# Optimization experiments

Hardware: AMD Instinct MI355X
Metric: run time of the kernel (lower is better)

The kernel has to match this reference:

```python
import jax, jax.numpy as jnp
import numpy as np

PRE_NMS_THRESH = 0.05
PRE_NMS_TOP_N = 200
NMS_THRESH = 0.5
FPN_POST_NMS_TOP_N = 100
MIN_SIZE = 0.0
NUM_CLASSES = 2
C = NUM_CLASSES - 1
NB = 2
STRIDES = (8, 16, 32, 64, 128)
HS = (100, 50, 25, 13, 7)
WS = (128, 64, 32, 16, 8)
IMG_H, IMG_W = 800, 1024
MAXV = 8  # max #vertices of quad-clipped-by-quad polygon


def _shoelace_fixed(V, n):
    # area of polygon stored in fixed buffer V[MAXV,2] with n valid vertices
    a = jnp.asarray(0.0, V.dtype)
    for k in range(MAXV):
        nxt = jnp.where(jnp.equal(k, n - 1), 0, k + 1)
        term = V[k, 0] * V[nxt, 1] - V[nxt, 0] * V[k, 1]
        a = a + jnp.where(k < n, term, 0.0)
    return 0.5 * jnp.abs(a)


def _quad_area(Q):  # Q: [4,2]
    x, y = Q[:, 0], Q[:, 1]
    return 0.5 * jnp.abs(jnp.sum(x * jnp.roll(y, -1) - jnp.roll(x, -1) * y))


def _clip_halfplane(V, n, p1, p2, orient):
    # Sutherland-Hodgman clip of polygon (V,n) against directed edge p1->p2
    d = p2 - p1

    def side(p):
        return orient * (d[0] * (p[1] - p1[1]) - d[1] * (p[0] - p1[0]))

    out = jnp.zeros((MAXV, 2), V.dtype)
    cnt = jnp.int32(0)
    for k in range(MAXV):
        cur = V[k]
        prev = V[jnp.where(jnp.equal(k, 0), n - 1, k - 1)]
        sc = side(cur)
        sp = side(prev)
        cur_in = sc >= 0.0
        prev_in = sp >= 0.0
        denom = sp - sc
        t = sp / jnp.where(jnp.abs(denom) > 1e-9, denom, 1e-9)
        ip = prev + t * (cur - prev)
        valid = k < n
        emit_ip = valid & (cur_in != prev_in)
        out = jnp.where(emit_ip, out.at[cnt].set(ip, mode='drop'), out)
        cnt = cnt + emit_ip.astype(jnp.int32)
        emit_cur = valid & cur_in
        out = jnp.where(emit_cur, out.at[cnt].set(cur, mode='drop'), out)
        cnt = cnt + emit_cur.astype(jnp.int32)
    return out, cnt


def _poly_inter_area(A, B):  # A,B: [4,2] convex quads
    sB = jnp.sum(B[:, 0] * jnp.roll(B[:, 1], -1) - jnp.roll(B[:, 0], -1) * B[:, 1])
    orient = jnp.where(sB >= 0.0, 1.0, -1.0)
    V = jnp.zeros((MAXV, 2), A.dtype).at[:4].set(A)
    n = jnp.int32(4)
    for e in range(4):
        V, n = _clip_halfplane(V, n, B[e], B[(e + 1) % 4], orient)
    return _shoelace_fixed(V, n)


def _process_level(loc, cls_l, reg_l, image_sizes):
    Nb, Cc, H, W = cls_l.shape
    # (N,C,H,W) -> (N,HW*C) with index = (h*W+w)*C + c (matches permute/reshape)
    scores = jax.nn.sigmoid(cls_l.transpose(0, 2, 3, 1).reshape(Nb, H * W * Cc))
    cand = scores > PRE_NMS_THRESH
    masked = jnp.where(cand, scores, 0.0)
    k = min(PRE_NMS_TOP_N, H * W * Cc)
    vals, idx = jax.lax.top_k(masked, k)
    loc_idx = idx // Cc
    labels = idx % Cc + 1
    regr = reg_l.transpose(0, 2, 3, 1).reshape(Nb, H * W, 8)
    reg_g = jnp.take_along_axis(regr, loc_idx[..., None], axis=1)  # [Nb,k,8]
    loc_g = loc[loc_idx]  # [Nb,k,2]
    poly = jnp.tile(loc_g, (1, 1, 4)) - reg_g  # (x-r0, y-r1, ..., x-r6, y-r7)
    hh = image_sizes[:, 0].astype(poly.dtype)[:, None, None]
    ww = image_sizes[:, 1].astype(poly.dtype)[:, None, None]
    xs = jnp.clip(poly[..., 0::2], 0.0, ww - 1.0)
    ys = jnp.clip(poly[..., 1::2], 0.0, hh - 1.0)
    poly = jnp.stack([xs, ys], axis=-1).reshape(Nb, k, 8)
    valid = vals > PRE_NMS_THRESH
    bw = xs.max(-1) - xs.min(-1)
    bh = ys.max(-1) - ys.min(-1)
    valid = valid & (bw >= MIN_SIZE) & (bh >= MIN_SIZE)
    sc = jnp.where(valid, jnp.sqrt(vals), 0.0)
    return poly, sc, labels, valid


def _nms_single(poly, scores, labels, valid):
    T = scores.shape[0]
    order = jnp.argsort(-scores)
    poly = poly[order]
    scores = scores[order]
    labels = labels[order]
    valid = valid[order]
    quads = poly.reshape(T, 4, 2)

    def pairwise_iou(q):
        inter = jax.vmap(jax.vmap(_poly_inter_area, (None, 0)), (0, None))(q, q)
        areas = jax.vmap(_quad_area)(q)
        union = areas[:, None] + areas[None, :] - inter
        return inter / jnp.maximum(union, 1e-9)

    # IoU only feeds boolean suppression decisions -> no gradient flows through it
    iou = jax.lax.stop_gradient(pairwise_iou(quads))
    ar = jnp.arange(T)

    def body(i, keep):
        sup = (iou[i] > NMS_THRESH) & (ar > i)
        return jnp.where(keep[i], keep & ~sup, keep)

    keep = jax.lax.stop_gradient(jax.lax.fori_loop(0, T, body, valid))
    final = jnp.where(keep, scores, -1.0)
    top_s, top_i = jax.lax.top_k(final, FPN_POST_NMS_TOP_N)
    ok = top_s > 0.0
    return poly[top_i], jnp.where(ok, top_s, 0.0), labels[top_i], ok


def _forward(locs, clss, regs, image_sizes):
    parts = [_process_level(l, c, r, image_sizes) for l, c, r in zip(locs, clss, regs)]
    poly = jnp.concatenate([p[0] for p in parts], axis=1)
    sc = jnp.concatenate([p[1] for p in parts], axis=1)
    lab = jnp.concatenate([p[2] for p in parts], axis=1)
    val = jnp.concatenate([p[3] for p in parts], axis=1)
    return jax.vmap(_nms_single)(poly, sc, lab, val)


def setup_inputs() -> dict:
    key = jax.random.key(0)
    inp = {}
    k = key
    for i, (h, w, s) in enumerate(zip(HS, WS, STRIDES)):
        k, k1, k2, k3 = jax.random.split(k, 4)
        sx = jnp.arange(w, dtype=jnp.float32) * s + s // 2
        sy = jnp.arange(h, dtype=jnp.float32) * s + s // 2
        yy, xx = jnp.meshgrid(sy, sx, indexing='ij')
        inp[f'locations_l{i}'] = jnp.stack([xx.reshape(-1), yy.reshape(-1)], axis=1)
        inp[f'box_cls_l{i}'] = jax.random.normal(k1, (NB, C, h, w), dtype=jnp.float32)
        inp[f'box_reg_l{i}'] = jax.random.normal(k2, (NB, 8, h, w), dtype=jnp.float32) * (2.0 * s)
        inp[f'centerness_l{i}'] = jax.random.normal(k3, (NB, 1, h, w), dtype=jnp.float32)
    inp['image_sizes'] = jnp.array([[IMG_H, IMG_W]] * NB, dtype=jnp.int32)
    return inp


def reference(locations_l0, locations_l1, locations_l2, locations_l3, locations_l4,
              box_cls_l0, box_cls_l1, box_cls_l2, box_cls_l3, box_cls_l4,
              box_reg_l0, box_reg_l1, box_reg_l2, box_reg_l3, box_reg_l4,
              centerness_l0, centerness_l1, centerness_l2, centerness_l3, centerness_l4,
              image_sizes):
    # centerness is accepted but unused, matching the original module's forward
    locs = [locations_l0, locations_l1, locations_l2, locations_l3, locations_l4]
    clss = [box_cls_l0, box_cls_l1, box_cls_l2, box_cls_l3, box_cls_l4]
    regs = [box_reg_l0, box_reg_l1, box_reg_l2, box_reg_l3, box_reg_l4]
    boxes, scores, labels, valid = _forward(locs, clss, regs, image_sizes)
    return boxes, scores, labels, valid
```

## Files before the change

### kernel.cpp

```cpp
#include <hip/hip_runtime.h>

#pragma clang fp contract(off)

#define T_CAND 856
#define NW 14
#define BSC 128
#define NSH 16
#define HSTR 513

__device__ const int d_HW[5]  = {12800, 3200, 800, 208, 56};
__device__ const int d_K[5]   = {200, 200, 200, 200, 56};
__device__ const int d_OFF[5] = {0, 200, 400, 600, 800};

struct LevelPtrs {
  const float* loc[5];
  const float* cls[5];
  const float* reg[5];
  const int*   img;
};

__device__ __forceinline__ unsigned long long readlane64(unsigned long long v, int lane) {
  const unsigned lo = (unsigned)__builtin_amdgcn_readlane((int)(unsigned)(v & 0xFFFFFFFFULL), lane);
  const unsigned hi = (unsigned)__builtin_amdgcn_readlane((int)(unsigned)(v >> 32), lane);
  return ((unsigned long long)hi << 32) | lo;
}
__device__ __forceinline__ unsigned long long rfl64(unsigned long long v) {
  const unsigned lo = (unsigned)__builtin_amdgcn_readfirstlane((int)(unsigned)(v & 0xFFFFFFFFULL));
  const unsigned hi = (unsigned)__builtin_amdgcn_readfirstlane((int)(unsigned)(v >> 32));
  return ((unsigned long long)hi << 32) | lo;
}

__global__ __launch_bounds__(1024) void topk_kernel(LevelPtrs P,
    float* __restrict__ candPoly, float* __restrict__ candSc, unsigned* __restrict__ candValid) {
  __shared__ unsigned hist[NSH * HSTR];
  __shared__ unsigned histT[512];
  __shared__ __align__(16) unsigned long long gbuf[1024];
  __shared__ int gcount;
  __shared__ int cutB;
  const int blk = blockIdx.x;
  const int b = blk / 5, l = blk % 5;
  const int HW = d_HW[l], K = d_K[l], OFF = d_OFF[l];
  const float* cls = P.cls[l] + (size_t)b * HW;
  const float* reg = P.reg[l] + (size_t)b * 8 * HW;
  const float* loc = P.loc[l];
  const int tid = threadIdx.x;

  for (int t = tid; t < NSH * HSTR; t += 1024) hist[t] = 0u;
  if (tid == 0) gcount = 0;
  __syncthreads();

  const int sh = (tid >> 2) & (NSH - 1);
  for (int idx = tid; idx < HW; idx += 1024) {
    const float x = cls[idx];
    const float s = (float)(1.0 / (1.0 + exp(-(double)x)));
    const float m = (s > 0.05f) ? s : 0.0f;
    atomicAdd(&hist[sh * HSTR + (__float_as_uint(m) >> 21)], 1u);
  }
  __syncthreads();
  for (int t = tid; t < 512; t += 1024) {
    unsigned sum = 0;
#pragma unroll
    for (int h = 0; h < NSH; ++h) sum += hist[h * HSTR + t];
    histT[t] = sum;
  }
  __syncthreads();
  if (tid == 0) {
    int acc = 0, bx = 511;
    for (; bx >= 0; --bx) { acc += (int)histT[bx]; if (acc >= K) break; }
    cutB = (bx < 0) ? 0 : bx;
  }
  __syncthreads();

  const int cb = cutB;
  for (int idx = tid; idx < HW; idx += 1024) {
    const float x = cls[idx];
    const float s = (float)(1.0 / (1.0 + exp(-(double)x)));
    const float m = (s > 0.05f) ? s : 0.0f;
    const unsigned kb = __float_as_uint(m);
    if ((int)(kb >> 21) >= cb) {
      const int pos = atomicAdd(&gcount, 1);
      if (pos < 1024)
        gbuf[pos] = ((unsigned long long)kb << 32)
                  | (unsigned long long)(0xFFFFFFFFu - (unsigned)idx);
    }
  }
  __syncthreads();
  const int G = min(gcount, 1024);
  if (tid < 4 && G + tid < 1024) gbuf[G + tid] = 0ULL;
  __syncthreads();

  if (tid < G) {
    const unsigned long long my = gbuf[tid];
    const int G4 = (G + 3) & ~3;
    int rank = 0;
    const ulonglong2* g2 = (const ulonglong2*)gbuf;
    for (int j = 0; j < G4 / 2; j += 2) {
      const ulonglong2 a = g2[j], c = g2[j + 1];
      rank += (a.x > my) ? 1 : 0;
      rank += (a.y > my) ? 1 : 0;
      rank += (c.x > my) ? 1 : 0;
      rank += (c.y > my) ? 1 : 0;
    }
    if (rank < K) {
      const float val = __uint_as_float((unsigned)(my >> 32));
      const int idx = (int)(0xFFFFFFFFu - (unsigned)(my & 0xFFFFFFFFULL));
      const float hh = (float)P.img[b * 2 + 0];
      const float ww = (float)P.img[b * 2 + 1];
      const float xmax = ww - 1.0f, ymax = hh - 1.0f;
      const float lx = loc[idx * 2 + 0], ly = loc[idx * 2 + 1];
      const int go = b * T_CAND + OFF + rank;
#pragma unroll
      for (int q = 0; q < 4; ++q) {
        const float rx = reg[(2 * q + 0) * HW + idx];
        const float ry = reg[(2 * q + 1) * HW + idx];
        const float pxv = fminf(fmaxf(lx - rx, 0.0f), xmax);
        const float pyv = fminf(fmaxf(ly - ry, 0.0f), ymax);
        candPoly[go * 8 + 2 * q + 0] = pxv;
        candPoly[go * 8 + 2 * q + 1] = pyv;
      }
      const bool v = (val > 0.05f);
      candSc[go]    = v ? sqrtf(val) : 0.0f;
      candValid[go] = v ? 1u : 0u;
    }
  }
}

__global__ __launch_bounds__(1024) void sort_kernel(
    const float* __restrict__ candPoly, const float* __restrict__ candSc,
    const unsigned* __restrict__ candValid,
    float* __restrict__ sPoly, float* __restrict__ sSc, unsigned* __restrict__ sValid) {
  __shared__ __align__(16) unsigned long long key[T_CAND];
  const int b = blockIdx.x, tid = threadIdx.x;
  float sc = 0.0f;
  if (tid < T_CAND) {
    sc = candSc[b * T_CAND + tid];
    key[tid] = ((unsigned long long)__float_as_uint(sc) << 32)
             | (unsigned long long)(0xFFFFFFFFu - (unsigned)tid);
  }
  __syncthreads();
  if (tid < T_CAND) {
    const unsigned long long my = key[tid];
    int rank = 0;
    const ulonglong2* k2 = (const ulonglong2*)key;
    for (int j = 0; j < T_CAND / 2; j += 2) {
      const ulonglong2 a = k2[j], c = k2[j + 1];
      rank += (a.x > my) ? 1 : 0;
      rank += (a.y > my) ? 1 : 0;
      rank += (c.x > my) ? 1 : 0;
      rank += (c.y > my) ? 1 : 0;
    }
    sSc[b * T_CAND + rank]    = sc;
    sValid[b * T_CAND + rank] = candValid[b * T_CAND + tid];
    const float4* src = (const float4*)(candPoly + (size_t)(b * T_CAND + tid) * 8);
    float4* dst = (float4*)(sPoly + (size_t)(b * T_CAND + rank) * 8);
    dst[0] = src[0];
    dst[1] = src[1];
  }
}

__global__ __launch_bounds__(BSC) void iou_kernel(const float* __restrict__ sPoly,
                                                  const unsigned* __restrict__ sValid,
                                                  unsigned long long* __restrict__ MT) {
  __shared__ float VX[2][8][BSC];
  __shared__ float VY[2][8][BSC];
  const int i = blockIdx.y, b = blockIdx.z;
  const int tid = threadIdx.x;
  if (blockIdx.x * BSC + (BSC - 1) <= (unsigned)i) {
    if ((tid & 63) == 0) {
      const int jw = blockIdx.x * (BSC / 64) + (tid >> 6);
      MT[((size_t)b * NW + jw) * T_CAND + i] = 0ULL;
    }
    return;
  }
  if (sValid[b * T_CAND + i] == 0u) return;
  const int j = blockIdx.x * BSC + tid;
  const float4* Ap4 = (const float4*)(sPoly + (size_t)(b * T_CAND + i) * 8);
  const float4 a01 = Ap4[0], a23 = Ap4[1];
  const float ax0 = a01.x, ay0 = a01.y, ax1 = a01.z, ay1 = a01.w,
              ax2 = a23.x, ay2 = a23.y, ax3 = a23.z, ay3 = a23.w;
  const int jc = (j < T_CAND) ? j : (T_CAND - 1);
  const float4* Bp4 = (const float4*)(sPoly + (size_t)(b * T_CAND + jc) * 8);
  const float4 b01 = Bp4[0], b23 = Bp4[1];
  const float bx0 = b01.x, by0 = b01.y, bx1 = b01.z, by1 = b01.w,
              bx2 = b23.x, by2 = b23.y, bx3 = b23.z, by3 = b23.w;
  const bool need = (j > i) && (j < T_CAND) && (sValid[b * T_CAND + jc] != 0u);
  const float aminx = fminf(fminf(ax0, ax1), fminf(ax2, ax3));
  const float amaxx = fmaxf(fmaxf(ax0, ax1), fmaxf(ax2, ax3));
  const float aminy = fminf(fminf(ay0, ay1), fminf(ay2, ay3));
  const float amaxy = fmaxf(fmaxf(ay0, ay1), fmaxf(ay2, ay3));
  const float bminx = fminf(fminf(bx0, bx1), fminf(bx2, bx3));
  const float bmaxx = fmaxf(fmaxf(bx0, bx1), fmaxf(bx2, bx3));
  const float bminy = fminf(fminf(by0, by1), fminf(by2, by3));
  const float bmaxy = fmaxf(fmaxf(by0, by1), fmaxf(by2, by3));
  const bool ov = !(amaxx < bminx || bmaxx < aminx || amaxy < bminy || bmaxy < aminy);
  bool hit = false;
  if (need && ov) {
    float sB = bx0 * by1 - bx1 * by0;
    sB += bx1 * by2 - bx2 * by1;
    sB += bx2 * by3 - bx3 * by2;
    sB += bx3 * by0 - bx0 * by3;
    const float orient = (sB >= 0.0f) ? 1.0f : -1.0f;

    VX[0][0][tid] = ax0; VY[0][0][tid] = ay0;
    VX[0][1][tid] = ax1; VY[0][1][tid] = ay1;
    VX[0][2][tid] = ax2; VY[0][2][tid] = ay2;
    VX[0][3][tid] = ax3; VY[0][3][tid] = ay3;
    int n = 4;
    const float bex[5] = {bx0, bx1, bx2, bx3, bx0};
    const float bey[5] = {by0, by1, by2, by3, by0};
#pragma unroll
    for (int e = 0; e < 4; ++e) {
      const int src = e & 1, dst = src ^ 1;
      const float p1x = bex[e], p1y = bey[e];
      const float dx = bex[e + 1] - p1x, dy = bey[e + 1] - p1y;
      int cnt = 0;
      int pidx = n - 1;
      pidx = pidx < 0 ? 0 : (pidx > 7 ? 7 : pidx);
      float px = VX[src][pidx][tid], py = VY[src][pidx][tid];
      float sp = orient * (dx * (py - p1y) - dy * (px - p1x));
#pragma unroll
      for (int k = 0; k < 8; ++k) {
        const float cx = VX[src][k][tid], cy = VY[src][k][tid];
        const float sc2 = orient * (dx * (cy - p1y) - dy * (cx - p1x));
        const bool cin = (sc2 >= 0.0f), pin = (sp >= 0.0f);
        const float denom = sp - sc2;
        const float dd = (fabsf(denom) > 1e-9f) ? denom : 1e-9f;
        const float t = sp / dd;
        const float ipx = px + t * (cx - px);
        const float ipy = py + t * (cy - py);
        const bool vk = (k < n);
        const bool e1 = vk && (cin != pin);
        if (e1 && cnt < 8) { VX[dst][cnt][tid] = ipx; VY[dst][cnt][tid] = ipy; }
        cnt += e1 ? 1 : 0;
        const bool e2 = vk && cin;
        if (e2 && cnt < 8) { VX[dst][cnt][tid] = cx; VY[dst][cnt][tid] = cy; }
        cnt += e2 ? 1 : 0;
        px = cx; py = cy; sp = sc2;
      }
      n = cnt;
    }
    float a = 0.0f;
#pragma unroll
    for (int k = 0; k < 8; ++k) {
      int nxt = (k == n - 1) ? 0 : ((k + 1 > 7) ? 7 : (k + 1));
      const float xk = VX[0][k][tid], yk = VY[0][k][tid];
      const float xn = VX[0][nxt][tid], yn = VY[0][nxt][tid];
      const float term = xk * yn - xn * yk;
      a += (k < n) ? term : 0.0f;
    }
    const float inter = 0.5f * fabsf(a);
    float aA = ax0 * ay1 - ax1 * ay0;
    aA += ax1 * ay2 - ax2 * ay1;
    aA += ax2 * ay3 - ax3 * ay2;
    aA += ax3 * ay0 - ax0 * ay3;
    const float areaA = 0.5f * fabsf(aA);
    const float areaB = 0.5f * fabsf(sB);
    const float uni = areaA + areaB - inter;
    const float iou = inter / fmaxf(uni, 1e-9f);
    hit = iou > 0.5f;
  }
  const unsigned long long ball = __ballot(hit);
  if ((tid & 63) == 0) {
    const int jw = blockIdx.x * (BSC / 64) + (tid >> 6);
    MT[((size_t)b * NW + jw) * T_CAND + i] = ball;
  }
}

__global__ __launch_bounds__(1024) void nms_resolve_kernel(const unsigned long long* __restrict__ MT,
    const unsigned* __restrict__ sValid, unsigned long long* __restrict__ kwOut) {
  __shared__ __align__(16) unsigned long long mt[NW * T_CAND];
  __shared__ unsigned long long vb[16];
  const int b = blockIdx.x;
  const int tid = threadIdx.x;
  const int wave = tid >> 6, lane = tid & 63;

  {
    const ulonglong2* g2 = (const ulonglong2*)(MT + (size_t)b * NW * T_CAND);
    ulonglong2* l2 = (ulonglong2*)mt;
    for (int t = tid; t < NW * T_CAND / 2; t += 1024) l2[t] = g2[t];
  }
  if (wave < NW) {
    const int idx = wave * 64 + lane;
    const bool v = (idx < T_CAND) && (sValid[b * T_CAND + idx] != 0u);
    const unsigned long long ball = __ballot(v);
    if (lane == 0) vb[wave] = ball;
  }
  __syncthreads();

  if (wave == 0) {
    unsigned long long kwreg = 0ULL;
    for (int q = 0; q < NW; ++q) {
      const unsigned long long* col = &mt[q * T_CAND];
      const int nrow = q * 64 + lane;
      const unsigned long long sup = col[nrow < T_CAND ? nrow : (T_CAND - 1)];
      unsigned long long acc = 0ULL;
      for (int wp = 0; wp < q; ++wp) {
        const unsigned long long row = col[wp * 64 + lane];
        const unsigned long long kword = readlane64(kwreg, wp);
        acc |= ((kword >> lane) & 1ULL) ? row : 0ULL;
      }
#pragma unroll
      for (int m = 1; m < 64; m <<= 1)
        acc |= (unsigned long long)__shfl_xor((long long)acc, m, 64);
      const unsigned long long S = rfl64(acc);
      const unsigned long long validq = rfl64(vb[q]);
      unsigned long long alive = validq & ~S;
      const unsigned long long suppr = __ballot(sup != 0ULL);
      unsigned long long rem = alive & suppr;
      while (rem) {
        const int s = (int)__builtin_ctzll(rem);
        rem &= rem - 1;
        if ((alive >> s) & 1ULL) {
          alive &= ~readlane64(sup, s);
          rem &= alive;
        }
      }
      if (lane == q) kwreg = alive;
    }
    if (lane < NW) kwOut[b * NW + lane] = kwreg;
  }
}

__global__ __launch_bounds__(128) void nms_emit_kernel(const unsigned long long* __restrict__ kwOut,
    const float* __restrict__ sPoly, const float* __restrict__ sSc, float* __restrict__ out) {
  const int b = blockIdx.x, tid = threadIdx.x;
  __shared__ unsigned long long kw[NW];
  if (tid < NW) kw[tid] = kwOut[b * NW + tid];
  __syncthreads();
  if (tid < 100) {
    const int o = tid;
    int totalKeep = 0;
    for (int w = 0; w < NW; ++w) totalKeep += __popcll(kw[w]);
    const bool kept = o < totalKeep;
    int idx = 0;
    if (kept) {
      int r = o, w = 0;
      unsigned long long word = 0ULL;
      for (; w < NW; ++w) {
        word = kw[w];
        const int c = __popcll(word);
        if (r < c) break;
        r -= c;
      }
      for (int p = 0; p < r; ++p) word &= word - 1;
      idx = w * 64 + (__ffsll(word) - 1);
    } else {
      int r = o - totalKeep, w = 0;
      unsigned long long word = 0ULL;
      for (; w < NW; ++w) {
        const unsigned long long mk = (w == NW - 1) ? ((1ULL << (T_CAND - 64 * (NW - 1))) - 1ULL)
                                                    : ~0ULL;
        word = (~kw[w]) & mk;
        const int c = __popcll(word);
        if (r < c) break;
        r -= c;
      }
      for (int p = 0; p < r; ++p) word &= word - 1;
      idx = w * 64 + (__ffsll(word) - 1);
    }
    const float4* pp = (const float4*)(sPoly + (size_t)(b * T_CAND + idx) * 8);
    float4* ob2 = (float4*)(out + (size_t)b * 800 + (size_t)o * 8);
    ob2[0] = pp[0];
    ob2[1] = pp[1];
    out[1600 + b * 100 + o] = kept ? sSc[b * T_CAND + idx] : 0.0f;
    out[1800 + b * 100 + o] = 1.0f;
    out[2000 + b * 100 + o] = kept ? 1.0f : 0.0f;
  }
}

extern "C" void kernel_launch(void* const* d_in, const int* in_sizes, int n_in,
                              void* d_out, int out_size, void* d_ws, size_t ws_size,
                              hipStream_t stream) {
  (void)n_in; (void)out_size; (void)ws_size;
  LevelPtrs P;
  const bool interleaved = (in_sizes[2] == 204800);
  for (int l = 0; l < 5; ++l) {
    if (interleaved) {
      P.loc[l] = (const float*)d_in[4 * l + 0];
      P.cls[l] = (const float*)d_in[4 * l + 1];
      P.reg[l] = (const float*)d_in[4 * l + 2];
    } else {
      P.loc[l] = (const float*)d_in[l];
      P.cls[l] = (const float*)d_in[5 + l];
      P.reg[l] = (const float*)d_in[10 + l];
    }
  }
  P.img = (const int*)d_in[20];

  char* ws = (char*)d_ws;
  float*    candPoly  = (float*)(ws + 0);
  float*    candSc    = (float*)(ws + 54784);
  unsigned* candValid = (unsigned*)(ws + 61632);
  float*    sPoly     = (float*)(ws + 68480);
  float*    sSc       = (float*)(ws + 123264);
  unsigned* sValid    = (unsigned*)(ws + 130112);
  unsigned long long* MT = (unsigned long long*)(ws + 136960);
  unsigned long long* kwOut = (unsigned long long*)(ws + 328704);

  topk_kernel<<<dim3(10), dim3(1024), 0, stream>>>(P, candPoly, candSc, candValid);
  sort_kernel<<<dim3(2), dim3(1024), 0, stream>>>(candPoly, candSc, candValid, sPoly, sSc, sValid);
  iou_kernel<<<dim3(7, T_CAND, 2), dim3(BSC), 0, stream>>>(sPoly, sValid, MT);
  nms_resolve_kernel<<<dim3(2), dim3(1024), 0, stream>>>(MT, sValid, kwOut);
  nms_emit_kernel<<<dim3(2), dim3(128), 0, stream>>>(kwOut, sPoly, sSc, (float*)d_out);
}
```

Measured before the change: 79.96 us.

## Compact AABB-overlapping pairs before polygon clipping and fuse NMS resolve with emit

Precomputes per-candidate AABBs during sort, then a tile kernel tests AABB overlap and writes a compacted list of candidate pairs. A grid-stride clip kernel runs Sutherland-Hodgman only on those pairs and sets suppression bits with atomicOr. The old dense iou grid did the clip work per lane and wasted SIMD on non-overlapping pairs. It also caches sigmoid scores in shared memory in topk to avoid a second exp pass, and merges resolve and emit into one launch. The price is an extra launch, global atomics, and an unbounded pair list in the workspace.

```diff
diff --git a/kernel.cpp b/kernel.cpp
--- a/kernel.cpp
+++ b/kernel.cpp
@@ -4,7 +4,6 @@
 
 #define T_CAND 856
 #define NW 14
-#define BSC 128
 #define NSH 16
 #define HSTR 513
 
@@ -35,6 +34,7 @@
   __shared__ unsigned hist[NSH * HSTR];
   __shared__ unsigned histT[512];
   __shared__ __align__(16) unsigned long long gbuf[1024];
+  __shared__ float mcache[12800];
   __shared__ int gcount;
   __shared__ int cutB;
   const int blk = blockIdx.x;
@@ -54,6 +54,7 @@
     const float x = cls[idx];
     const float s = (float)(1.0 / (1.0 + exp(-(double)x)));
     const float m = (s > 0.05f) ? s : 0.0f;
+    mcache[idx] = m;
     atomicAdd(&hist[sh * HSTR + (__float_as_uint(m) >> 21)], 1u);
   }
   __syncthreads();
@@ -73,10 +74,7 @@
 
   const int cb = cutB;
   for (int idx = tid; idx < HW; idx += 1024) {
-    const float x = cls[idx];
-    const float s = (float)(1.0 / (1.0 + exp(-(double)x)));
-    const float m = (s > 0.05f) ? s : 0.0f;
-    const unsigned kb = __float_as_uint(m);
+    const unsigned kb = __float_as_uint(mcache[idx]);
     if ((int)(kb >> 21) >= cb) {
       const int pos = atomicAdd(&gcount, 1);
       if (pos < 1024)
@@ -128,9 +126,11 @@
 __global__ __launch_bounds__(1024) void sort_kernel(
     const float* __restrict__ candPoly, const float* __restrict__ candSc,
     const unsigned* __restrict__ candValid,
-    float* __restrict__ sPoly, float* __restrict__ sSc, unsigned* __restrict__ sValid) {
+    float* __restrict__ sPoly, float* __restrict__ sSc, unsigned* __restrict__ sValid,
+    float* __restrict__ sAABB, unsigned* __restrict__ pairCount) {
   __shared__ __align__(16) unsigned long long key[T_CAND];
   const int b = blockIdx.x, tid = threadIdx.x;
+  if (b == 0 && tid == 0) *pairCount = 0u;
   float sc = 0.0f;
   if (tid < T_CAND) {
     sc = candSc[b * T_CAND + tid];
@@ -152,49 +152,87 @@
     sSc[b * T_CAND + rank]    = sc;
     sValid[b * T_CAND + rank] = candValid[b * T_CAND + tid];
     const float4* src = (const float4*)(candPoly + (size_t)(b * T_CAND + tid) * 8);
+    const float4 s0 = src[0], s1 = src[1];
     float4* dst = (float4*)(sPoly + (size_t)(b * T_CAND + rank) * 8);
-    dst[0] = src[0];
-    dst[1] = src[1];
-  }
-}
-
-__global__ __launch_bounds__(BSC) void iou_kernel(const float* __restrict__ sPoly,
-                                                  const unsigned* __restrict__ sValid,
-                                                  unsigned long long* __restrict__ MT) {
-  __shared__ float VX[2][8][BSC];
-  __shared__ float VY[2][8][BSC];
-  const int i = blockIdx.y, b = blockIdx.z;
+    dst[0] = s0;
+    dst[1] = s1;
+    float4 bb;
+    bb.x = fminf(fminf(s0.x, s0.z), fminf(s1.x, s1.z));
+    bb.y = fminf(fminf(s0.y, s0.w), fminf(s1.y, s1.w));
+    bb.z = fmaxf(fmaxf(s0.x, s0.z), fmaxf(s1.x, s1.z));
+    bb.w = fmaxf(fmaxf(s0.y, s0.w), fmaxf(s1.y, s1.w));
+    *(float4*)(sAABB + (size_t)(b * T_CAND + rank) * 4) = bb;
+  }
+}
+
+__global__ __launch_bounds__(64) void aabb_pairs_kernel(
+    const float* __restrict__ sAABB, const unsigned* __restrict__ sValid,
+    unsigned long long* __restrict__ MT, unsigned* __restrict__ pairList,
+    unsigned* __restrict__ pairCount) {
+  const int jt = blockIdx.x, it = blockIdx.y, b = blockIdx.z;
+  const int lane = threadIdx.x;
+  const int iRow = it * 64 + lane;
+  if (jt < it) {
+    if (iRow < T_CAND) MT[((size_t)b * NW + jt) * T_CAND + iRow] = 0ULL;
+    return;
+  }
+  const int j = jt * 64 + lane;
+  const int jc = j < T_CAND ? j : T_CAND - 1;
+  const float4 jb = *(const float4*)(sAABB + (size_t)(b * T_CAND + jc) * 4);
+  const bool jv = (j < T_CAND) && (sValid[b * T_CAND + j] != 0u);
+  const int ic = iRow < T_CAND ? iRow : T_CAND - 1;
+  const float4 ib = *(const float4*)(sAABB + (size_t)(b * T_CAND + ic) * 4);
+  const int iv = (iRow < T_CAND) && (sValid[b * T_CAND + ic] != 0u);
+  unsigned long long roww = 0ULL;
+  for (int q = 0; q < 64; ++q) {
+    const float iminx = __shfl(ib.x, q), iminy = __shfl(ib.y, q);
+    const float imaxx = __shfl(ib.z, q), imaxy = __shfl(ib.w, q);
+    const int ivq = __shfl(iv, q);
+    const int irow_q = it * 64 + q;
+    const bool ov = !(imaxx < jb.x || jb.z < iminx || imaxy < jb.y || jb.w < iminy);
+    const bool pred = ivq && jv && (j > irow_q) && ov;
+    const unsigned long long w = __ballot(pred);
+    if (lane == q) roww = w;
+  }
+  if (iRow < T_CAND) MT[((size_t)b * NW + jt) * T_CAND + iRow] = 0ULL;
+  const int cnt = __popcll(roww);
+  int incl = cnt;
+#pragma unroll
+  for (int d = 1; d < 64; d <<= 1) {
+    const int v = __shfl_up(incl, d);
+    if (lane >= d) incl += v;
+  }
+  const int ex = incl - cnt;
+  int base = 0;
+  if (lane == 63) base = (int)atomicAdd(pairCount, (unsigned)incl);
+  base = __shfl(base, 63);
+  unsigned off = (unsigned)(base + ex);
+  unsigned long long t = roww;
+  while (t) {
+    const int jb2 = (int)__builtin_ctzll(t);
+    t &= t - 1;
+    pairList[off++] = ((unsigned)b << 20) | ((unsigned)iRow << 10) | (unsigned)(jt * 64 + jb2);
+  }
+}
+
+__global__ __launch_bounds__(256) void clip_kernel(
+    const unsigned* __restrict__ pairList, const unsigned* __restrict__ pairCount,
+    const float* __restrict__ sPoly, unsigned long long* __restrict__ MT) {
+  __shared__ float VX[2][8][256];
+  __shared__ float VY[2][8][256];
   const int tid = threadIdx.x;
-  if (blockIdx.x * BSC + (BSC - 1) <= (unsigned)i) {
-    if ((tid & 63) == 0) {
-      const int jw = blockIdx.x * (BSC / 64) + (tid >> 6);
-      MT[((size_t)b * NW + jw) * T_CAND + i] = 0ULL;
-    }
-    return;
-  }
-  if (sValid[b * T_CAND + i] == 0u) return;
-  const int j = blockIdx.x * BSC + tid;
-  const float4* Ap4 = (const float4*)(sPoly + (size_t)(b * T_CAND + i) * 8);
-  const float4 a01 = Ap4[0], a23 = Ap4[1];
-  const float ax0 = a01.x, ay0 = a01.y, ax1 = a01.z, ay1 = a01.w,
-              ax2 = a23.x, ay2 = a23.y, ax3 = a23.z, ay3 = a23.w;
-  const int jc = (j < T_CAND) ? j : (T_CAND - 1);
-  const float4* Bp4 = (const float4*)(sPoly + (size_t)(b * T_CAND + jc) * 8);
-  const float4 b01 = Bp4[0], b23 = Bp4[1];
-  const float bx0 = b01.x, by0 = b01.y, bx1 = b01.z, by1 = b01.w,
-              bx2 = b23.x, by2 = b23.y, bx3 = b23.z, by3 = b23.w;
-  const bool need = (j > i) && (j < T_CAND) && (sValid[b * T_CAND + jc] != 0u);
-  const float aminx = fminf(fminf(ax0, ax1), fminf(ax2, ax3));
-  const float amaxx = fmaxf(fmaxf(ax0, ax1), fmaxf(ax2, ax3));
-  const float aminy = fminf(fminf(ay0, ay1), fminf(ay2, ay3));
-  const float amaxy = fmaxf(fmaxf(ay0, ay1), fmaxf(ay2, ay3));
-  const float bminx = fminf(fminf(bx0, bx1), fminf(bx2, bx3));
-  const float bmaxx = fmaxf(fmaxf(bx0, bx1), fmaxf(bx2, bx3));
-  const float bminy = fminf(fminf(by0, by1), fminf(by2, by3));
-  const float bmaxy = fmaxf(fmaxf(by0, by1), fmaxf(by2, by3));
-  const bool ov = !(amaxx < bminx || bmaxx < aminx || amaxy < bminy || bmaxy < aminy);
-  bool hit = false;
-  if (need && ov) {
+  const unsigned count = *pairCount;
+  for (unsigned t0 = blockIdx.x * 256 + tid; t0 < count; t0 += gridDim.x * 256) {
+    const unsigned pk = pairList[t0];
+    const int b = (pk >> 20) & 1, i = (pk >> 10) & 1023, j = pk & 1023;
+    const float4* Ap4 = (const float4*)(sPoly + (size_t)(b * T_CAND + i) * 8);
+    const float4 a01 = Ap4[0], a23 = Ap4[1];
+    const float ax0 = a01.x, ay0 = a01.y, ax1 = a01.z, ay1 = a01.w,
+                ax2 = a23.x, ay2 = a23.y, ax3 = a23.z, ay3 = a23.w;
+    const float4* Bp4 = (const float4*)(sPoly + (size_t)(b * T_CAND + j) * 8);
+    const float4 b01 = Bp4[0], b23 = Bp4[1];
+    const float bx0 = b01.x, by0 = b01.y, bx1 = b01.z, by1 = b01.w,
+                bx2 = b23.x, by2 = b23.y, bx3 = b23.z, by3 = b23.w;
     float sB = bx0 * by1 - bx1 * by0;
     sB += bx1 * by2 - bx2 * by1;
     sB += bx2 * by3 - bx3 * by2;
@@ -218,8 +256,8 @@
       pidx = pidx < 0 ? 0 : (pidx > 7 ? 7 : pidx);
       float px = VX[src][pidx][tid], py = VY[src][pidx][tid];
       float sp = orient * (dx * (py - p1y) - dy * (px - p1x));
-#pragma unroll
       for (int k = 0; k < 8; ++k) {
+        if (k >= n) break;
         const float cx = VX[src][k][tid], cy = VY[src][k][tid];
         const float sc2 = orient * (dx * (cy - p1y) - dy * (cx - p1x));
         const bool cin = (sc2 >= 0.0f), pin = (sp >= 0.0f);
@@ -228,25 +266,22 @@
         const float t = sp / dd;
         const float ipx = px + t * (cx - px);
         const float ipy = py + t * (cy - py);
-        const bool vk = (k < n);
-        const bool e1 = vk && (cin != pin);
+        const bool e1 = (cin != pin);
         if (e1 && cnt < 8) { VX[dst][cnt][tid] = ipx; VY[dst][cnt][tid] = ipy; }
         cnt += e1 ? 1 : 0;
-        const bool e2 = vk && cin;
-        if (e2 && cnt < 8) { VX[dst][cnt][tid] = cx; VY[dst][cnt][tid] = cy; }
-        cnt += e2 ? 1 : 0;
+        if (cin && cnt < 8) { VX[dst][cnt][tid] = cx; VY[dst][cnt][tid] = cy; }
+        cnt += cin ? 1 : 0;
         px = cx; py = cy; sp = sc2;
       }
       n = cnt;
     }
     float a = 0.0f;
-#pragma unroll
     for (int k = 0; k < 8; ++k) {
-      int nxt = (k == n - 1) ? 0 : ((k + 1 > 7) ? 7 : (k + 1));
+      if (k >= n) break;
+      const int nxt = (k == n - 1) ? 0 : ((k + 1 > 7) ? 7 : (k + 1));
       const float xk = VX[0][k][tid], yk = VY[0][k][tid];
       const float xn = VX[0][nxt][tid], yn = VY[0][nxt][tid];
-      const float term = xk * yn - xn * yk;
-      a += (k < n) ? term : 0.0f;
+      a += xk * yn - xn * yk;
     }
     const float inter = 0.5f * fabsf(a);
     float aA = ax0 * ay1 - ax1 * ay0;
@@ -257,19 +292,17 @@
     const float areaB = 0.5f * fabsf(sB);
     const float uni = areaA + areaB - inter;
     const float iou = inter / fmaxf(uni, 1e-9f);
-    hit = iou > 0.5f;
-  }
-  const unsigned long long ball = __ballot(hit);
-  if ((tid & 63) == 0) {
-    const int jw = blockIdx.x * (BSC / 64) + (tid >> 6);
-    MT[((size_t)b * NW + jw) * T_CAND + i] = ball;
-  }
-}
-
-__global__ __launch_bounds__(1024) void nms_resolve_kernel(const unsigned long long* __restrict__ MT,
-    const unsigned* __restrict__ sValid, unsigned long long* __restrict__ kwOut) {
+    if (iou > 0.5f)
+      atomicOr(&MT[((size_t)b * NW + (j >> 6)) * T_CAND + i], 1ULL << (j & 63));
+  }
+}
+
+__global__ __launch_bounds__(1024) void nms_resolve_emit_kernel(
+    const unsigned long long* __restrict__ MT, const unsigned* __restrict__ sValid,
+    const float* __restrict__ sPoly, const float* __restrict__ sSc, float* __restrict__ out) {
   __shared__ __align__(16) unsigned long long mt[NW * T_CAND];
   __shared__ unsigned long long vb[16];
+  __shared__ unsigned long long kw[NW];
   const int b = blockIdx.x;
   const int tid = threadIdx.x;
   const int wave = tid >> 6, lane = tid & 63;
@@ -317,16 +350,10 @@
       }
       if (lane == q) kwreg = alive;
     }
-    if (lane < NW) kwOut[b * NW + lane] = kwreg;
-  }
-}
-
-__global__ __launch_bounds__(128) void nms_emit_kernel(const unsigned long long* __restrict__ kwOut,
-    const float* __restrict__ sPoly, const float* __restrict__ sSc, float* __restrict__ out) {
-  const int b = blockIdx.x, tid = threadIdx.x;
-  __shared__ unsigned long long kw[NW];
-  if (tid < NW) kw[tid] = kwOut[b * NW + tid];
-  __syncthreads();
+    if (lane < NW) kw[lane] = kwreg;
+  }
+  __syncthreads();
+
   if (tid < 100) {
     const int o = tid;
     int totalKeep = 0;
@@ -395,11 +422,16 @@
   float*    sSc       = (float*)(ws + 123264);
   unsigned* sValid    = (unsigned*)(ws + 130112);
   unsigned long long* MT = (unsigned long long*)(ws + 136960);
-  unsigned long long* kwOut = (unsigned long long*)(ws + 328704);
+  float*    sAABB     = (float*)(ws + 328704);
+  unsigned* pairCount = (unsigned*)(ws + 356096);
+  unsigned* pairList  = (unsigned*)(ws + 356112);
 
   topk_kernel<<<dim3(10), dim3(1024), 0, stream>>>(P, candPoly, candSc, candValid);
-  sort_kernel<<<dim3(2), dim3(1024), 0, stream>>>(candPoly, candSc, candValid, sPoly, sSc, sValid);
-  iou_kernel<<<dim3(7, T_CAND, 2), dim3(BSC), 0, stream>>>(sPoly, sValid, MT);
-  nms_resolve_kernel<<<dim3(2), dim3(1024), 0, stream>>>(MT, sValid, kwOut);
-  nms_emit_kernel<<<dim3(2), dim3(128), 0, stream>>>(kwOut, sPoly, sSc, (float*)d_out);
-}
+  sort_kernel<<<dim3(2), dim3(1024), 0, stream>>>(candPoly, candSc, candValid,
+                                                  sPoly, sSc, sValid, sAABB, pairCount);
+  aabb_pairs_kernel<<<dim3(NW, NW, 2), dim3(64), 0, stream>>>(sAABB, sValid, MT,
+                                                              pairList, pairCount);
+  clip_kernel<<<dim3(512), dim3(256), 0, stream>>>(pairList, pairCount, sPoly, MT);
+  nms_resolve_emit_kernel<<<dim3(2), dim3(1024), 0, stream>>>(MT, sValid, sPoly, sSc,
+                                                              (float*)d_out);
+}
```

Result: faster. 75.11 us (-6.1%).
